# Performance work log

Measured on AMD Instinct MI355X. Metric: run time of the kernel, lower is better.

Reference implementation:

```python
import jax, jax.numpy as jnp
import numpy as np

H = 1024
E = 8
TOP_K = 2


def setup_inputs() -> dict:
    key = jax.random.key(0)
    ks = jax.random.split(key, 6)
    B, S = 4, 2048
    hidden_states = jax.random.normal(ks[0], (B, S, H), dtype=jnp.float32)
    # router weight, init N(0, 0.02)
    router_w = jax.random.normal(ks[1], (E, H), dtype=jnp.float32) * 0.02
    # stacked expert FFN params (nn.Linear: y = x @ W.T + b)
    lim = 1.0 / np.sqrt(H)
    W1 = jax.random.uniform(ks[2], (E, H, H), minval=-lim, maxval=lim, dtype=jnp.float32)
    b1 = jax.random.uniform(ks[3], (E, H), minval=-lim, maxval=lim, dtype=jnp.float32)
    W2 = jax.random.uniform(ks[4], (E, H, H), minval=-lim, maxval=lim, dtype=jnp.float32)
    b2 = jax.random.uniform(ks[5], (E, H), minval=-lim, maxval=lim, dtype=jnp.float32)
    return {"hidden_states": hidden_states, "router_w": router_w,
            "W1": W1, "b1": b1, "W2": W2, "b2": b2}


def reference(hidden_states, router_w, W1, b1, W2, b2):
    B, S, _ = hidden_states.shape
    # ---- router ----
    logits = jnp.einsum('bsh,eh->bse', hidden_states, router_w)  # [B,S,E]
    router_probs = jax.nn.softmax(logits.astype(jnp.float32), axis=-1)
    top_vals, top_idx = jax.lax.top_k(router_probs, TOP_K)        # [B,S,K]
    top_vals = top_vals / jnp.sum(top_vals, axis=-1, keepdims=True)  # norm_topk_prob
    # per-token per-expert combine weight (sum of top-k weights matching expert)
    w = jnp.sum(jax.nn.one_hot(top_idx, E, dtype=top_vals.dtype) * top_vals[..., None], axis=-2)  # [B,S,E]
    # ---- dense all-expert FFN (faithful to reference: every expert on every token) ----
    h1 = jax.nn.relu(jnp.einsum('bsh,efh->bsef', hidden_states, W1) + b1)   # [B,S,E,F]
    expert_out = jnp.einsum('bsef,egf->bseg', h1, W2) + b2                  # [B,S,E,H]
    moe_out = jnp.einsum('bseh,bse->bsh', expert_out, w)
    return hidden_states + moe_out, router_probs
```

## Files before the change

### kernel.cpp

```cpp
#include <hip/hip_runtime.h>
#include <hip/hip_bf16.h>


#define HD   1024
#define NTOK 8192
#define NEXP 8
#define BM   128
#define BN   128
#define BK   64
#define ZROW 8192
#define MAXP 17408
#define EP_LDSW 136

typedef __attribute__((ext_vector_type(8))) short  vshort8;
typedef __attribute__((ext_vector_type(4))) short  vshort4;
typedef __attribute__((ext_vector_type(4))) float  vfloat4;

typedef __attribute__((address_space(1))) const unsigned gas_uint;
typedef __attribute__((address_space(3))) unsigned       las_uint;

__device__ __forceinline__ void gld16(const void* g, void* l) {
    __builtin_amdgcn_global_load_lds((gas_uint*)g, (las_uint*)l, 16, 0, 0);
}

__device__ __forceinline__ short bf16r(float f) {
    union { float f; unsigned u; } a; a.f = f;
    unsigned r = a.u + 0x7FFFu + ((a.u >> 16) & 1u);
    return (short)(r >> 16);
}

__global__ void init_kernel(int* counts, int* fill, int* pair_token, short* xb) {
    int i = blockIdx.x * 256 + threadIdx.x;
    if (i < NEXP) { counts[i] = 0; fill[i] = 0; }
    if (i < MAXP) pair_token[i] = ZROW;
    if (i < HD / 8) {
        vshort8 z = {0, 0, 0, 0, 0, 0, 0, 0};
        *(vshort8*)(xb + (size_t)ZROW * HD + i * 8) = z;
    }
}

__global__ __launch_bounds__(256) void router_kernel(
    const float* __restrict__ x, const float* __restrict__ rw,
    float* __restrict__ out, short* __restrict__ xb,
    float* __restrict__ probs_out, int2* __restrict__ tok_top,
    float2* __restrict__ tok_w, int* __restrict__ counts) {
    __shared__ float rws[NEXP * HD];
    __shared__ int hist[NEXP];
    int t = threadIdx.x;
    if (t < NEXP) hist[t] = 0;
    for (int j = 0; j < 8; ++j) {
        int idx = j * 1024 + t * 4;
        *(vfloat4*)(rws + idx) = *(const vfloat4*)(rw + idx);
    }
    __syncthreads();
    int wave = t >> 6, lane = t & 63;
    for (int it = 0; it < 8; ++it) {
        int token = blockIdx.x * 32 + it * 4 + wave;
        const float* xr = x + (size_t)token * HD;
        float part[NEXP];
#pragma unroll
        for (int e = 0; e < NEXP; ++e) part[e] = 0.f;
        for (int j = 0; j < 4; ++j) {
            int off = j * 256 + lane * 4;
            vfloat4 xv = *(const vfloat4*)(xr + off);
            *(vfloat4*)(out + (size_t)token * HD + off) = xv;
            vshort4 bq;
            bq.x = bf16r(xv.x); bq.y = bf16r(xv.y); bq.z = bf16r(xv.z); bq.w = bf16r(xv.w);
            *(vshort4*)(xb + (size_t)token * HD + off) = bq;
#pragma unroll
            for (int e = 0; e < NEXP; ++e) {
                vfloat4 wv = *(const vfloat4*)(rws + e * HD + off);
                part[e] += xv.x * wv.x + xv.y * wv.y + xv.z * wv.z + xv.w * wv.w;
            }
        }
#pragma unroll
        for (int e = 0; e < NEXP; ++e)
            for (int off = 32; off; off >>= 1)
                part[e] += __shfl_xor(part[e], off, 64);
        if (lane == 0) {
            float m = part[0];
#pragma unroll
            for (int e = 1; e < NEXP; ++e) m = fmaxf(m, part[e]);
            float p[NEXP], s = 0.f;
#pragma unroll
            for (int e = 0; e < NEXP; ++e) { p[e] = expf(part[e] - m); s += p[e]; }
            float inv = 1.f / s;
#pragma unroll
            for (int e = 0; e < NEXP; ++e) {
                p[e] *= inv;
                probs_out[(size_t)token * NEXP + e] = p[e];
            }
            int i0 = 0;
#pragma unroll
            for (int e = 1; e < NEXP; ++e) if (p[e] > p[i0]) i0 = e;
            int i1 = (i0 == 0) ? 1 : 0;
#pragma unroll
            for (int e = 0; e < NEXP; ++e) if (e != i0 && p[e] > p[i1]) i1 = e;
            float s2 = 1.f / (p[i0] + p[i1]);
            tok_top[token] = make_int2(i0, i1);
            tok_w[token]   = make_float2(p[i0] * s2, p[i1] * s2);
            atomicAdd(&hist[i0], 1);
            atomicAdd(&hist[i1], 1);
        }
    }
    __syncthreads();
    if (t < NEXP) atomicAdd(&counts[t], hist[t]);
}

__global__ __launch_bounds__(256) void scatter_kernel(
    const int2* __restrict__ tok_top, const float2* __restrict__ tok_w,
    const int* __restrict__ counts, int* fill,
    int* __restrict__ pair_token, float* __restrict__ pair_w) {
    __shared__ int lhist[NEXP];
    __shared__ int lbase[NEXP];
    int t = threadIdx.x;
    if (t < NEXP) lhist[t] = 0;
    __syncthreads();
    int offs[NEXP];
    {
        int acc = 0;
#pragma unroll
        for (int f = 0; f < NEXP; ++f) {
            offs[f] = acc;
            acc += (counts[f] + 127) & ~127;
        }
    }
    int token = blockIdx.x * 256 + t;
    int2 ti = tok_top[token];
    float2 tw = tok_w[token];
    int r0 = atomicAdd(&lhist[ti.x], 1);
    int r1 = atomicAdd(&lhist[ti.y], 1);
    __syncthreads();
    if (t < NEXP) lbase[t] = atomicAdd(&fill[t], lhist[t]);
    __syncthreads();
    int s0 = offs[ti.x] + lbase[ti.x] + r0;
    pair_token[s0] = token; pair_w[s0] = tw.x;
    int s1 = offs[ti.y] + lbase[ti.y] + r1;
    pair_token[s1] = token; pair_w[s1] = tw.y;
}

__global__ void convw_kernel(const float* __restrict__ W1, const float* __restrict__ W2,
                             short* __restrict__ D1, short* __restrict__ D2) {
    size_t t = (size_t)blockIdx.x * 256 + threadIdx.x;
    const size_t PER = (size_t)NEXP * HD * HD / 8;
    const float* src = W1; short* dst = D1;
    if (t >= PER) { t -= PER; src = W2; dst = D2; }
    size_t C = t >> 6;
    int l  = (int)(t & 63);
    int kc = (int)(C & 31);
    int ng = (int)((C >> 5) & 63);
    int ei = (int)(C >> 11);
    int n = ng * 16 + (l & 15);
    int k = kc * 32 + (l >> 4) * 8;
    const float* s = src + ((size_t)ei * HD + n) * HD + k;
    vfloat4 a = *(const vfloat4*)s;
    vfloat4 b = *(const vfloat4*)(s + 4);
    vshort8 o;
    o[0] = bf16r(a.x); o[1] = bf16r(a.y); o[2] = bf16r(a.z); o[3] = bf16r(a.w);
    o[4] = bf16r(b.x); o[5] = bf16r(b.y); o[6] = bf16r(b.z); o[7] = bf16r(b.w);
    *(vshort8*)(dst + t * 8) = o;
}

template <int MODE>
__global__ __launch_bounds__(512, 4) void moe_gemm(
    const short* __restrict__ A, const short* __restrict__ Bw,
    const float* __restrict__ bias, const int* __restrict__ pair_token,
    const float* __restrict__ pair_w, const int* __restrict__ counts,
    short* __restrict__ h1sw_out, float* __restrict__ out) {
    __shared__ short smem[32768];

    const int row0 = blockIdx.x * BM;
    int e = 0;
    {
        int csum = 0;
#pragma unroll
        for (int f = 0; f < NEXP; ++f) {
            int p = (counts[f] + 127) & ~127;
            if (csum + p <= row0) e = f + 1;
            csum += p;
        }
        if (row0 >= csum) return;
    }

    const int t = threadIdx.x;
    const int wave = t >> 6, lane = t & 63;
    const int wm = wave >> 2, wn = wave & 3;
    const int quad = lane >> 4, l16 = lane & 15;
    const int colb = blockIdx.y * BN;

    const char* agp;
    if (MODE == 0) {
        int tok = pair_token[row0 + wave * 16 + l16];
        agp = (const char*)A + (size_t)tok * (HD * 2) + quad * 16;
    } else {
        agp = (const char*)A + (((size_t)(row0 >> 4) + wave) * 32) * 1024 + lane * 16;
    }
    const char* bgp = (const char*)Bw +
        (((size_t)e * 64 + (colb >> 4) + wave) * 32) * 1024 + lane * 16;

    vfloat4 acc[4][2];
#pragma unroll
    for (int i = 0; i < 4; ++i)
#pragma unroll
        for (int j = 0; j < 2; ++j)
            acc[i][j] = (vfloat4){0.f, 0.f, 0.f, 0.f};

#define STAGE(bsel, kk0)                                                      \
    {                                                                         \
        const int kc_ = (kk0) >> 5;                                           \
        short* sa_ = smem + (bsel) * 8192;                                    \
        short* sb_ = smem + 16384 + (bsel) * 8192;                            \
        _Pragma("unroll")                                                     \
        for (int s = 0; s < 2; ++s) {                                         \
            const char* ga_ = (MODE == 0)                                     \
                ? (agp + (size_t)(kk0) * 2 + s * 64)                          \
                : (agp + (size_t)(kc_ + s) * 1024);                           \
            gld16(ga_, sa_ + (wave * 2 + s) * 512);                           \
            gld16(bgp + (size_t)(kc_ + s) * 1024, sb_ + (wave * 2 + s) * 512);\
        }                                                                     \
    }

    STAGE(0, 0)
    int cur = 0;
    for (int kt = 0; kt < HD / BK; ++kt) {
        if (kt < HD / BK - 1) {
            STAGE(cur ^ 1, (kt + 1) * BK)
            asm volatile("s_waitcnt vmcnt(4)" ::: "memory");
        } else {
            asm volatile("s_waitcnt vmcnt(0)" ::: "memory");
        }
        __builtin_amdgcn_s_barrier();
        asm volatile("" ::: "memory");
        const short* sa = smem + cur * 8192;
        const short* sb = smem + 16384 + cur * 8192;
#pragma unroll
        for (int s = 0; s < 2; ++s) {
            vshort8 af[4], bfr[2];
#pragma unroll
            for (int i = 0; i < 4; ++i)
                af[i] = *(const vshort8*)(sa + ((wm * 4 + i) * 2 + s) * 512 + lane * 8);
#pragma unroll
            for (int j = 0; j < 2; ++j)
                bfr[j] = *(const vshort8*)(sb + ((wn * 2 + j) * 2 + s) * 512 + lane * 8);
#pragma unroll
            for (int i = 0; i < 4; ++i)
#pragma unroll
                for (int j = 0; j < 2; ++j)
                    acc[i][j] = __builtin_amdgcn_mfma_f32_16x16x32_bf16(af[i], bfr[j], acc[i][j], 0, 0, 0);
        }
        asm volatile("" ::: "memory");
        __builtin_amdgcn_s_barrier();
        cur ^= 1;
    }
#undef STAGE

    if (MODE == 0) {
        __syncthreads();
#pragma unroll
        for (int j = 0; j < 2; ++j) {
            int col = wn * 32 + j * 16 + l16;
            float bv = bias[e * HD + colb + col];
#pragma unroll
            for (int i = 0; i < 4; ++i) {
                int rl = wm * 64 + i * 16 + quad * 4;
#pragma unroll
                for (int reg = 0; reg < 4; ++reg) {
                    float v = acc[i][j][reg] + bv;
                    v = v > 0.f ? v : 0.f;
                    smem[(rl + reg) * EP_LDSW + col] = bf16r(v);
                }
            }
        }
        __syncthreads();
        int lrow = wave * 16 + l16;
#pragma unroll
        for (int kk = 0; kk < 4; ++kk) {
            vshort8 v = *(const vshort8*)(smem + lrow * EP_LDSW + kk * 32 + quad * 8);
            size_t chunk = ((size_t)((row0 >> 4) + wave) * 32) + ((colb >> 5) + kk);
            *(vshort8*)(h1sw_out + chunk * 512 + lane * 8) = v;
        }
    } else {
        int tok[4][4]; float wv[4][4];
#pragma unroll
        for (int i = 0; i < 4; ++i)
#pragma unroll
            for (int reg = 0; reg < 4; ++reg) {
                int r = row0 + wm * 64 + i * 16 + quad * 4 + reg;
                tok[i][reg] = pair_token[r];
                wv[i][reg] = pair_w[r];
            }
#pragma unroll
        for (int j = 0; j < 2; ++j) {
            int col = colb + wn * 32 + j * 16 + l16;
            float bv = bias[e * HD + col];
#pragma unroll
            for (int i = 0; i < 4; ++i)
#pragma unroll
                for (int reg = 0; reg < 4; ++reg)
                    if (tok[i][reg] < ZROW)
                        atomicAdd(out + (size_t)tok[i][reg] * HD + col,
                                  wv[i][reg] * (acc[i][j][reg] + bv));
        }
    }
}

extern "C" void kernel_launch(void* const* d_in, const int* in_sizes, int n_in,
                              void* d_out, int out_size, void* d_ws, size_t ws_size,
                              hipStream_t stream) {
    const float* x  = (const float*)d_in[0];
    const float* rw = (const float*)d_in[1];
    const float* W1 = (const float*)d_in[2];
    const float* b1 = (const float*)d_in[3];
    const float* W2 = (const float*)d_in[4];
    const float* b2 = (const float*)d_in[5];
    float* out   = (float*)d_out;
    float* probs = out + (size_t)NTOK * HD;

    char* ws = (char*)d_ws;
    short* xb = (short*)ws;            ws += (size_t)(NTOK + 1) * HD * 2;
    short* h1 = (short*)ws;            ws += (size_t)MAXP * HD * 2;
    int*   pair_token = (int*)ws;      ws += MAXP * 4;
    float* pair_w     = (float*)ws;    ws += MAXP * 4;
    int*   counts = (int*)ws;          ws += 256;
    int*   fill   = (int*)ws;          ws += 256;
    int2*   tok_top = (int2*)ws;       ws += NTOK * 8;
    float2* tok_w   = (float2*)ws;     ws += NTOK * 8;
    short* w1sw = (short*)ws;          ws += (size_t)NEXP * HD * HD * 2;
    short* w2sw = (short*)ws;          ws += (size_t)NEXP * HD * HD * 2;
    (void)ws_size;

    init_kernel<<<MAXP / 256, 256, 0, stream>>>(counts, fill, pair_token, xb);
    router_kernel<<<NTOK / 32, 256, 0, stream>>>(x, rw, out, xb, probs,
                                                 tok_top, tok_w, counts);
    scatter_kernel<<<NTOK / 256, 256, 0, stream>>>(tok_top, tok_w, counts, fill,
                                                   pair_token, pair_w);
    int cg = (int)(2 * ((size_t)NEXP * HD * HD / 8) / 256);
    convw_kernel<<<cg, 256, 0, stream>>>(W1, W2, w1sw, w2sw);
    dim3 gg(MAXP / BM, HD / BN);
    moe_gemm<0><<<gg, 512, 0, stream>>>(xb, w1sw, b1, pair_token, pair_w, counts, h1, nullptr);
    moe_gemm<1><<<gg, 512, 0, stream>>>(h1, w2sw, b2, pair_token, pair_w, counts, nullptr, out);
}
```

Measured before the change: 311.5 us.

## Widen GEMM tile to 128x256 with BK=32 and two-pass epilogue

Doubles the N-dimension of each block tile to 256 and halves the K step to 32, so each wave computes a 64x64 sub-tile (4x4 MFMAs) instead of 64x32. The aim is more MFMA work per LDS fragment load and fewer blocks re-reading the A tile, with slightly less LDS per block. The MODE 0 epilogue now writes the wider tile in two halves through the same LDS staging buffer. The costs are higher accumulator register pressure, which may reduce occupancy under the launch bound, and twice as many K iterations and barriers.

```diff
diff --git a/kernel.cpp b/kernel.cpp
--- a/kernel.cpp
+++ b/kernel.cpp
@@ -6,8 +6,8 @@
 #define NTOK 8192
 #define NEXP 8
 #define BM   128
-#define BN   128
-#define BK   64
+#define BN   256
+#define BK   32
 #define ZROW 8192
 #define MAXP 17408
 #define EP_LDSW 136
@@ -167,7 +167,7 @@
     const float* __restrict__ bias, const int* __restrict__ pair_token,
     const float* __restrict__ pair_w, const int* __restrict__ counts,
     short* __restrict__ h1sw_out, float* __restrict__ out) {
-    __shared__ short smem[32768];
+    __shared__ short smem[24576];
 
     const int row0 = blockIdx.x * BM;
     int e = 0;
@@ -193,61 +193,55 @@
         int tok = pair_token[row0 + wave * 16 + l16];
         agp = (const char*)A + (size_t)tok * (HD * 2) + quad * 16;
     } else {
-        agp = (const char*)A + (((size_t)(row0 >> 4) + wave) * 32) * 1024 + lane * 16;
+        agp = (const char*)A + ((size_t)(row0 >> 4) + wave) * 32768 + lane * 16;
     }
     const char* bgp = (const char*)Bw +
-        (((size_t)e * 64 + (colb >> 4) + wave) * 32) * 1024 + lane * 16;
-
-    vfloat4 acc[4][2];
+        ((size_t)e * 64 + (colb >> 4) + 2 * wave) * 32768 + lane * 16;
+
+    vfloat4 acc[4][4];
 #pragma unroll
     for (int i = 0; i < 4; ++i)
 #pragma unroll
-        for (int j = 0; j < 2; ++j)
+        for (int j = 0; j < 4; ++j)
             acc[i][j] = (vfloat4){0.f, 0.f, 0.f, 0.f};
 
-#define STAGE(bsel, kk0)                                                      \
+#define STAGE(bsel, kt_)                                                      \
     {                                                                         \
-        const int kc_ = (kk0) >> 5;                                           \
-        short* sa_ = smem + (bsel) * 8192;                                    \
-        short* sb_ = smem + 16384 + (bsel) * 8192;                            \
-        _Pragma("unroll")                                                     \
-        for (int s = 0; s < 2; ++s) {                                         \
-            const char* ga_ = (MODE == 0)                                     \
-                ? (agp + (size_t)(kk0) * 2 + s * 64)                          \
-                : (agp + (size_t)(kc_ + s) * 1024);                           \
-            gld16(ga_, sa_ + (wave * 2 + s) * 512);                           \
-            gld16(bgp + (size_t)(kc_ + s) * 1024, sb_ + (wave * 2 + s) * 512);\
-        }                                                                     \
+        short* sa_ = smem + (bsel) * 4096;                                    \
+        short* sb_ = smem + 8192 + (bsel) * 8192;                             \
+        const char* ga_ = (MODE == 0)                                         \
+            ? (agp + (size_t)(kt_) * 64)                                      \
+            : (agp + (size_t)(kt_) * 1024);                                   \
+        gld16(ga_, sa_ + wave * 512);                                         \
+        gld16(bgp + (size_t)(kt_) * 1024,         sb_ + (2 * wave) * 512);    \
+        gld16(bgp + 32768 + (size_t)(kt_) * 1024, sb_ + (2 * wave + 1) * 512);\
     }
 
     STAGE(0, 0)
     int cur = 0;
     for (int kt = 0; kt < HD / BK; ++kt) {
         if (kt < HD / BK - 1) {
-            STAGE(cur ^ 1, (kt + 1) * BK)
-            asm volatile("s_waitcnt vmcnt(4)" ::: "memory");
+            STAGE(cur ^ 1, kt + 1)
+            asm volatile("s_waitcnt vmcnt(3)" ::: "memory");
         } else {
             asm volatile("s_waitcnt vmcnt(0)" ::: "memory");
         }
         __builtin_amdgcn_s_barrier();
         asm volatile("" ::: "memory");
-        const short* sa = smem + cur * 8192;
-        const short* sb = smem + 16384 + cur * 8192;
-#pragma unroll
-        for (int s = 0; s < 2; ++s) {
-            vshort8 af[4], bfr[2];
-#pragma unroll
-            for (int i = 0; i < 4; ++i)
-                af[i] = *(const vshort8*)(sa + ((wm * 4 + i) * 2 + s) * 512 + lane * 8);
-#pragma unroll
-            for (int j = 0; j < 2; ++j)
-                bfr[j] = *(const vshort8*)(sb + ((wn * 2 + j) * 2 + s) * 512 + lane * 8);
-#pragma unroll
-            for (int i = 0; i < 4; ++i)
-#pragma unroll
-                for (int j = 0; j < 2; ++j)
-                    acc[i][j] = __builtin_amdgcn_mfma_f32_16x16x32_bf16(af[i], bfr[j], acc[i][j], 0, 0, 0);
-        }
+        const short* sa = smem + cur * 4096;
+        const short* sb = smem + 8192 + cur * 8192;
+        vshort8 af[4], bfr[4];
+#pragma unroll
+        for (int i = 0; i < 4; ++i)
+            af[i] = *(const vshort8*)(sa + (wm * 4 + i) * 512 + lane * 8);
+#pragma unroll
+        for (int j = 0; j < 4; ++j)
+            bfr[j] = *(const vshort8*)(sb + (wn * 4 + j) * 512 + lane * 8);
+#pragma unroll
+        for (int i = 0; i < 4; ++i)
+#pragma unroll
+            for (int j = 0; j < 4; ++j)
+                acc[i][j] = __builtin_amdgcn_mfma_f32_16x16x32_bf16(af[i], bfr[j], acc[i][j], 0, 0, 0);
         asm volatile("" ::: "memory");
         __builtin_amdgcn_s_barrier();
         cur ^= 1;
@@ -257,27 +251,33 @@
     if (MODE == 0) {
         __syncthreads();
 #pragma unroll
-        for (int j = 0; j < 2; ++j) {
-            int col = wn * 32 + j * 16 + l16;
-            float bv = bias[e * HD + colb + col];
-#pragma unroll
-            for (int i = 0; i < 4; ++i) {
-                int rl = wm * 64 + i * 16 + quad * 4;
-#pragma unroll
-                for (int reg = 0; reg < 4; ++reg) {
-                    float v = acc[i][j][reg] + bv;
-                    v = v > 0.f ? v : 0.f;
-                    smem[(rl + reg) * EP_LDSW + col] = bf16r(v);
+        for (int h = 0; h < 2; ++h) {
+            if ((wn >> 1) == h) {
+#pragma unroll
+                for (int j = 0; j < 4; ++j) {
+                    int col = (wn & 1) * 64 + j * 16 + l16;
+                    float bv = bias[e * HD + colb + h * 128 + col];
+#pragma unroll
+                    for (int i = 0; i < 4; ++i) {
+                        int rl = wm * 64 + i * 16 + quad * 4;
+#pragma unroll
+                        for (int reg = 0; reg < 4; ++reg) {
+                            float v = acc[i][j][reg] + bv;
+                            v = v > 0.f ? v : 0.f;
+                            smem[(rl + reg) * EP_LDSW + col] = bf16r(v);
+                        }
+                    }
                 }
             }
-        }
-        __syncthreads();
-        int lrow = wave * 16 + l16;
-#pragma unroll
-        for (int kk = 0; kk < 4; ++kk) {
-            vshort8 v = *(const vshort8*)(smem + lrow * EP_LDSW + kk * 32 + quad * 8);
-            size_t chunk = ((size_t)((row0 >> 4) + wave) * 32) + ((colb >> 5) + kk);
-            *(vshort8*)(h1sw_out + chunk * 512 + lane * 8) = v;
+            __syncthreads();
+            int lrow = wave * 16 + l16;
+#pragma unroll
+            for (int kk = 0; kk < 4; ++kk) {
+                vshort8 v = *(const vshort8*)(smem + lrow * EP_LDSW + kk * 32 + quad * 8);
+                size_t chunk = ((size_t)((row0 >> 4) + wave) * 32) + (colb >> 5) + h * 4 + kk;
+                *(vshort8*)(h1sw_out + chunk * 512 + lane * 8) = v;
+            }
+            if (h == 0) __syncthreads();
         }
     } else {
         int tok[4][4]; float wv[4][4];
@@ -290,8 +290,8 @@
                 wv[i][reg] = pair_w[r];
             }
 #pragma unroll
-        for (int j = 0; j < 2; ++j) {
-            int col = colb + wn * 32 + j * 16 + l16;
+        for (int j = 0; j < 4; ++j) {
+            int col = colb + wn * 64 + j * 16 + l16;
             float bv = bias[e * HD + col];
 #pragma unroll
             for (int i = 0; i < 4; ++i)
```

New measurement: 313.0 us. Within noise of the previous version (+0.5%).

## Fuse router, weight conversion and init into one kernel; remap GEMM grid

Applied to the files above, without the earlier changes.

Merges the init, router and weight bf16-conversion kernels into a single block-partitioned prep kernel, keeping only a tiny counter-zeroing launch before it. This removes launch gaps and lets the router overlap with the bandwidth-heavy weight conversion. The GEMM grid is also remapped so consecutive blocks cover all column tiles of the same row tile, improving L2 reuse of activation rows. The risk is heterogeneous block work in one launch.

```diff
diff --git a/kernel.cpp b/kernel.cpp
--- a/kernel.cpp
+++ b/kernel.cpp
@@ -29,82 +29,110 @@
     return (short)(r >> 16);
 }
 
-__global__ void init_kernel(int* counts, int* fill, int* pair_token, short* xb) {
-    int i = blockIdx.x * 256 + threadIdx.x;
-    if (i < NEXP) { counts[i] = 0; fill[i] = 0; }
-    if (i < MAXP) pair_token[i] = ZROW;
-    if (i < HD / 8) {
-        vshort8 z = {0, 0, 0, 0, 0, 0, 0, 0};
-        *(vshort8*)(xb + (size_t)ZROW * HD + i * 8) = z;
-    }
-}
-
-__global__ __launch_bounds__(256) void router_kernel(
+__global__ void zero_kernel(int* counts, int* fill) {
+    int t = threadIdx.x;
+    if (t < NEXP) { counts[t] = 0; fill[t] = 0; }
+}
+
+__global__ __launch_bounds__(256) void prep_kernel(
     const float* __restrict__ x, const float* __restrict__ rw,
     float* __restrict__ out, short* __restrict__ xb,
     float* __restrict__ probs_out, int2* __restrict__ tok_top,
-    float2* __restrict__ tok_w, int* __restrict__ counts) {
+    float2* __restrict__ tok_w, int* __restrict__ counts,
+    int* __restrict__ pair_token,
+    const float* __restrict__ W1, const float* __restrict__ W2,
+    short* __restrict__ D1, short* __restrict__ D2) {
     __shared__ float rws[NEXP * HD];
     __shared__ int hist[NEXP];
-    int t = threadIdx.x;
-    if (t < NEXP) hist[t] = 0;
-    for (int j = 0; j < 8; ++j) {
-        int idx = j * 1024 + t * 4;
-        *(vfloat4*)(rws + idx) = *(const vfloat4*)(rw + idx);
-    }
-    __syncthreads();
-    int wave = t >> 6, lane = t & 63;
-    for (int it = 0; it < 8; ++it) {
-        int token = blockIdx.x * 32 + it * 4 + wave;
-        const float* xr = x + (size_t)token * HD;
-        float part[NEXP];
-#pragma unroll
-        for (int e = 0; e < NEXP; ++e) part[e] = 0.f;
-        for (int j = 0; j < 4; ++j) {
-            int off = j * 256 + lane * 4;
-            vfloat4 xv = *(const vfloat4*)(xr + off);
-            *(vfloat4*)(out + (size_t)token * HD + off) = xv;
-            vshort4 bq;
-            bq.x = bf16r(xv.x); bq.y = bf16r(xv.y); bq.z = bf16r(xv.z); bq.w = bf16r(xv.w);
-            *(vshort4*)(xb + (size_t)token * HD + off) = bq;
-#pragma unroll
-            for (int e = 0; e < NEXP; ++e) {
-                vfloat4 wv = *(const vfloat4*)(rws + e * HD + off);
-                part[e] += xv.x * wv.x + xv.y * wv.y + xv.z * wv.z + xv.w * wv.w;
+    const int blk = blockIdx.x;
+    const int t = threadIdx.x;
+
+    if (blk < 256) {
+        if (t < NEXP) hist[t] = 0;
+        for (int j = 0; j < 8; ++j) {
+            int idx = j * 1024 + t * 4;
+            *(vfloat4*)(rws + idx) = *(const vfloat4*)(rw + idx);
+        }
+        __syncthreads();
+        int wave = t >> 6, lane = t & 63;
+        for (int it = 0; it < 8; ++it) {
+            int token = blk * 32 + it * 4 + wave;
+            const float* xr = x + (size_t)token * HD;
+            float part[NEXP];
+#pragma unroll
+            for (int e = 0; e < NEXP; ++e) part[e] = 0.f;
+            for (int j = 0; j < 4; ++j) {
+                int off = j * 256 + lane * 4;
+                vfloat4 xv = *(const vfloat4*)(xr + off);
+                *(vfloat4*)(out + (size_t)token * HD + off) = xv;
+                vshort4 bq;
+                bq.x = bf16r(xv.x); bq.y = bf16r(xv.y); bq.z = bf16r(xv.z); bq.w = bf16r(xv.w);
+                *(vshort4*)(xb + (size_t)token * HD + off) = bq;
+#pragma unroll
+                for (int e = 0; e < NEXP; ++e) {
+                    vfloat4 wv = *(const vfloat4*)(rws + e * HD + off);
+                    part[e] += xv.x * wv.x + xv.y * wv.y + xv.z * wv.z + xv.w * wv.w;
+                }
             }
-        }
-#pragma unroll
-        for (int e = 0; e < NEXP; ++e)
-            for (int off = 32; off; off >>= 1)
-                part[e] += __shfl_xor(part[e], off, 64);
-        if (lane == 0) {
-            float m = part[0];
-#pragma unroll
-            for (int e = 1; e < NEXP; ++e) m = fmaxf(m, part[e]);
-            float p[NEXP], s = 0.f;
-#pragma unroll
-            for (int e = 0; e < NEXP; ++e) { p[e] = expf(part[e] - m); s += p[e]; }
-            float inv = 1.f / s;
-#pragma unroll
-            for (int e = 0; e < NEXP; ++e) {
-                p[e] *= inv;
-                probs_out[(size_t)token * NEXP + e] = p[e];
+#pragma unroll
+            for (int e = 0; e < NEXP; ++e)
+                for (int off = 32; off; off >>= 1)
+                    part[e] += __shfl_xor(part[e], off, 64);
+            if (lane == 0) {
+                float m = part[0];
+#pragma unroll
+                for (int e = 1; e < NEXP; ++e) m = fmaxf(m, part[e]);
+                float p[NEXP], s = 0.f;
+#pragma unroll
+                for (int e = 0; e < NEXP; ++e) { p[e] = expf(part[e] - m); s += p[e]; }
+                float inv = 1.f / s;
+#pragma unroll
+                for (int e = 0; e < NEXP; ++e) {
+                    p[e] *= inv;
+                    probs_out[(size_t)token * NEXP + e] = p[e];
+                }
+                int i0 = 0;
+#pragma unroll
+                for (int e = 1; e < NEXP; ++e) if (p[e] > p[i0]) i0 = e;
+                int i1 = (i0 == 0) ? 1 : 0;
+#pragma unroll
+                for (int e = 0; e < NEXP; ++e) if (e != i0 && p[e] > p[i1]) i1 = e;
+                float s2 = 1.f / (p[i0] + p[i1]);
+                tok_top[token] = make_int2(i0, i1);
+                tok_w[token]   = make_float2(p[i0] * s2, p[i1] * s2);
+                atomicAdd(&hist[i0], 1);
+                atomicAdd(&hist[i1], 1);
             }
-            int i0 = 0;
-#pragma unroll
-            for (int e = 1; e < NEXP; ++e) if (p[e] > p[i0]) i0 = e;
-            int i1 = (i0 == 0) ? 1 : 0;
-#pragma unroll
-            for (int e = 0; e < NEXP; ++e) if (e != i0 && p[e] > p[i1]) i1 = e;
-            float s2 = 1.f / (p[i0] + p[i1]);
-            tok_top[token] = make_int2(i0, i1);
-            tok_w[token]   = make_float2(p[i0] * s2, p[i1] * s2);
-            atomicAdd(&hist[i0], 1);
-            atomicAdd(&hist[i1], 1);
-        }
-    }
-    __syncthreads();
-    if (t < NEXP) atomicAdd(&counts[t], hist[t]);
+        }
+        __syncthreads();
+        if (t < NEXP) atomicAdd(&counts[t], hist[t]);
+    } else if (blk < 8448) {
+        size_t tt = (size_t)(blk - 256) * 256 + t;
+        const size_t PER = (size_t)NEXP * HD * HD / 8;
+        const float* src = W1; short* dst = D1;
+        if (tt >= PER) { tt -= PER; src = W2; dst = D2; }
+        size_t C = tt >> 6;
+        int l  = (int)(tt & 63);
+        int kc = (int)(C & 31);
+        int ng = (int)((C >> 5) & 63);
+        int ei = (int)(C >> 11);
+        int n = ng * 16 + (l & 15);
+        int k = kc * 32 + (l >> 4) * 8;
+        const float* s = src + ((size_t)ei * HD + n) * HD + k;
+        vfloat4 a = *(const vfloat4*)s;
+        vfloat4 b = *(const vfloat4*)(s + 4);
+        vshort8 o;
+        o[0] = bf16r(a.x); o[1] = bf16r(a.y); o[2] = bf16r(a.z); o[3] = bf16r(a.w);
+        o[4] = bf16r(b.x); o[5] = bf16r(b.y); o[6] = bf16r(b.z); o[7] = bf16r(b.w);
+        *(vshort8*)(dst + tt * 8) = o;
+    } else {
+        int i = (blk - 8448) * 256 + t;
+        if (i < MAXP) pair_token[i] = ZROW;
+        if (i < HD / 8) {
+            vshort8 z = {0, 0, 0, 0, 0, 0, 0, 0};
+            *(vshort8*)(xb + (size_t)ZROW * HD + i * 8) = z;
+        }
+    }
 }
 
 __global__ __launch_bounds__(256) void scatter_kernel(
@@ -139,28 +167,6 @@
     pair_token[s1] = token; pair_w[s1] = tw.y;
 }
 
-__global__ void convw_kernel(const float* __restrict__ W1, const float* __restrict__ W2,
-                             short* __restrict__ D1, short* __restrict__ D2) {
-    size_t t = (size_t)blockIdx.x * 256 + threadIdx.x;
-    const size_t PER = (size_t)NEXP * HD * HD / 8;
-    const float* src = W1; short* dst = D1;
-    if (t >= PER) { t -= PER; src = W2; dst = D2; }
-    size_t C = t >> 6;
-    int l  = (int)(t & 63);
-    int kc = (int)(C & 31);
-    int ng = (int)((C >> 5) & 63);
-    int ei = (int)(C >> 11);
-    int n = ng * 16 + (l & 15);
-    int k = kc * 32 + (l >> 4) * 8;
-    const float* s = src + ((size_t)ei * HD + n) * HD + k;
-    vfloat4 a = *(const vfloat4*)s;
-    vfloat4 b = *(const vfloat4*)(s + 4);
-    vshort8 o;
-    o[0] = bf16r(a.x); o[1] = bf16r(a.y); o[2] = bf16r(a.z); o[3] = bf16r(a.w);
-    o[4] = bf16r(b.x); o[5] = bf16r(b.y); o[6] = bf16r(b.z); o[7] = bf16r(b.w);
-    *(vshort8*)(dst + t * 8) = o;
-}
-
 template <int MODE>
 __global__ __launch_bounds__(512, 4) void moe_gemm(
     const short* __restrict__ A, const short* __restrict__ Bw,
@@ -169,7 +175,11 @@
     short* __restrict__ h1sw_out, float* __restrict__ out) {
     __shared__ short smem[32768];
 
-    const int row0 = blockIdx.x * BM;
+    const int bx = blockIdx.x, by = blockIdx.y;
+    const int row_t = by * 17 + (bx >> 3);
+    const int col_t = bx & 7;
+
+    const int row0 = row_t * BM;
     int e = 0;
     {
         int csum = 0;
@@ -186,7 +196,7 @@
     const int wave = t >> 6, lane = t & 63;
     const int wm = wave >> 2, wn = wave & 3;
     const int quad = lane >> 4, l16 = lane & 15;
-    const int colb = blockIdx.y * BN;
+    const int colb = col_t * BN;
 
     const char* agp;
     if (MODE == 0) {
@@ -276,7 +286,7 @@
 #pragma unroll
         for (int kk = 0; kk < 4; ++kk) {
             vshort8 v = *(const vshort8*)(smem + lrow * EP_LDSW + kk * 32 + quad * 8);
-            size_t chunk = ((size_t)((row0 >> 4) + wave) * 32) + ((colb >> 5) + kk);
+            size_t chunk = ((size_t)(row0 >> 4) + wave) * 32 + (colb >> 5) + kk;
             *(vshort8*)(h1sw_out + chunk * 512 + lane * 8) = v;
         }
     } else {
@@ -329,14 +339,13 @@
     short* w2sw = (short*)ws;          ws += (size_t)NEXP * HD * HD * 2;
     (void)ws_size;
 
-    init_kernel<<<MAXP / 256, 256, 0, stream>>>(counts, fill, pair_token, xb);
-    router_kernel<<<NTOK / 32, 256, 0, stream>>>(x, rw, out, xb, probs,
-                                                 tok_top, tok_w, counts);
+    zero_kernel<<<1, 256, 0, stream>>>(counts, fill);
+    prep_kernel<<<8516, 256, 0, stream>>>(x, rw, out, xb, probs, tok_top, tok_w,
+                                          counts, pair_token,
+                                          W1, W2, w1sw, w2sw);
     scatter_kernel<<<NTOK / 256, 256, 0, stream>>>(tok_top, tok_w, counts, fill,
                                                    pair_token, pair_w);
-    int cg = (int)(2 * ((size_t)NEXP * HD * HD / 8) / 256);
-    convw_kernel<<<cg, 256, 0, stream>>>(W1, W2, w1sw, w2sw);
-    dim3 gg(MAXP / BM, HD / BN);
+    dim3 gg(136, 8);
     moe_gemm<0><<<gg, 512, 0, stream>>>(xb, w1sw, b1, pair_token, pair_w, counts, h1, nullptr);
     moe_gemm<1><<<gg, 512, 0, stream>>>(h1, w2sw, b2, pair_token, pair_w, counts, nullptr, out);
 }
```

After: 302.3 us. -3.0%, faster.
